# Performance work log

Hardware: AMD Instinct MI355X
Metric: run time of the kernel (lower is better)

## Reference

```python
import jax, jax.numpy as jnp
import numpy as np

N_HEAD = 16
SCALE = True  # module's scale flag: divides scores by d_head (as written, NOT sqrt)
NEG = 1e10


def setup_inputs() -> dict:
    key = jax.random.key(0)
    k0, k1, k2 = jax.random.split(key, 3)
    B, S, NX = 2, 2048, 1024
    x = jax.random.normal(k0, (B, S, NX), dtype=jnp.float32)
    w_attn = jax.random.normal(k1, (NX, 3 * NX), dtype=jnp.float32) * 0.02
    b_attn = jnp.zeros((3 * NX,), dtype=jnp.float32)
    w_proj = jax.random.normal(k2, (NX, NX), dtype=jnp.float32) * 0.02
    b_proj = jnp.zeros((NX,), dtype=jnp.float32)
    return {"x": x, "w_attn": w_attn, "b_attn": b_attn, "w_proj": w_proj, "b_proj": b_proj}


def reference(x, w_attn, b_attn, w_proj, b_proj):
    B, S, nx = x.shape
    d = nx // N_HEAD
    # c_attn: fused qkv projection (Conv1D == addmm)
    qkv = x @ w_attn + b_attn  # [B,S,3*nx]
    q, k, v = jnp.split(qkv, 3, axis=-1)

    def heads(t):
        return t.reshape(B, S, N_HEAD, d).transpose(0, 2, 1, 3)  # [B,H,S,d]

    q, k, v = heads(q), heads(k), heads(v)
    w = jnp.einsum('bhqd,bhkd->bhqk', q, k)  # [B,H,S,S]
    if SCALE:
        w = w / d  # module divides by v.size(-1) == d_head (not sqrt)
    mask = jnp.tril(jnp.ones((S, S), dtype=w.dtype))
    w = w * mask - NEG * (1.0 - mask)
    w = jax.nn.softmax(w, axis=-1)
    a = jnp.einsum('bhqk,bhkd->bhqd', w, v)
    a = a.transpose(0, 2, 1, 3).reshape(B, S, nx)  # merge_heads
    out = a @ w_proj + b_proj  # c_proj
    # present = stack(key.transpose(-2,-1), value); key was [B,H,d,S] in torch,
    # so stored key is [B,H,S,d] which equals our k.
    present = jnp.stack((k, v))  # [2,B,H,S,d]
    return out, present
```

## Files before the change

kernel.cpp:

```cpp
#include <hip/hip_runtime.h>
#include <hip/hip_bf16.h>
#include <stdint.h>


typedef __bf16 bf16;
typedef __attribute__((ext_vector_type(8))) __bf16 bf16x8;
typedef __attribute__((ext_vector_type(4))) float f32x4;

#define SEQ 2048
#define NXD 1024
#define DH 64
#define LP 72

__device__ __forceinline__ f32x4 mfma16(bf16x8 a, bf16x8 b, f32x4 c) {
  return __builtin_amdgcn_mfma_f32_16x16x32_bf16(a, b, c, 0, 0, 0);
}

__global__ __launch_bounds__(256) void convert_f32_bf16(
    const float* __restrict__ in, bf16* __restrict__ out, int n8) {
  const int i = blockIdx.x * 256 + threadIdx.x;
  if (i >= n8) return;
  const float4 a = ((const float4*)in)[i * 2];
  const float4 b = ((const float4*)in)[i * 2 + 1];
  bf16x8 o;
  o[0] = (bf16)a.x; o[1] = (bf16)a.y; o[2] = (bf16)a.z; o[3] = (bf16)a.w;
  o[4] = (bf16)b.x; o[5] = (bf16)b.y; o[6] = (bf16)b.z; o[7] = (bf16)b.w;
  ((bf16x8*)out)[i] = o;
}

__global__ __launch_bounds__(256) void transpose64_f2b(
    const float* __restrict__ in, bf16* __restrict__ out, int R, int C) {
  __shared__ bf16 tile[64 * 65];
  const int t = threadIdx.x;
  const size_t bofs = (size_t)blockIdx.z * R * C;
  const float* ib = in + bofs;
  bf16* ob = out + bofs;
  const int r0 = blockIdx.y * 64, c0 = blockIdx.x * 64;
#pragma unroll
  for (int i = 0; i < 4; i++) {
    int flat = (i * 256 + t) * 4;
    int row = flat >> 6, col = flat & 63;
    float4 v = *(const float4*)(ib + (size_t)(r0 + row) * C + c0 + col);
    tile[row * 65 + col + 0] = (bf16)v.x;
    tile[row * 65 + col + 1] = (bf16)v.y;
    tile[row * 65 + col + 2] = (bf16)v.z;
    tile[row * 65 + col + 3] = (bf16)v.w;
  }
  __syncthreads();
#pragma unroll
  for (int i = 0; i < 2; i++) {
    int flat = (i * 256 + t) * 8;
    int orow = flat >> 6, ocol = flat & 63;
    bf16x8 v;
#pragma unroll
    for (int e = 0; e < 8; e++) v[e] = tile[(ocol + e) * 65 + orow];
    *(bf16x8*)(ob + (size_t)(c0 + orow) * R + r0 + ocol) = v;
  }
}

template <int MODE>
__global__ __launch_bounds__(256) void gemm128s(
    const bf16* __restrict__ A, const bf16* __restrict__ BT,
    const float* __restrict__ bias, bf16* __restrict__ qb,
    float* __restrict__ of1, float* __restrict__ of2) {
  __shared__ bf16 As[128 * LP];
  __shared__ bf16 Bs[128 * LP];
  const int t = threadIdx.x;
  const int lane = t & 63, wave = t >> 6;
  const int hi = lane >> 4, ln = lane & 15;
  const int wr = wave >> 1, wc = wave & 1;
  const int tm0 = blockIdx.y * 128, tn0 = blockIdx.x * 128;

  f32x4 acc[4][4];
#pragma unroll
  for (int m = 0; m < 4; m++)
#pragma unroll
    for (int n = 0; n < 4; n++) acc[m][n] = (f32x4){0.f, 0.f, 0.f, 0.f};

  for (int k0 = 0; k0 < 1024; k0 += 64) {
#pragma unroll
    for (int it = 0; it < 4; ++it) {
      const int e = (it * 256 + t) * 8;
      const int row = e >> 6, col = e & 63;
      *(bf16x8*)(As + row * LP + col) =
          *(const bf16x8*)(A + (size_t)(tm0 + row) * 1024 + k0 + col);
      *(bf16x8*)(Bs + row * LP + col) =
          *(const bf16x8*)(BT + (size_t)(tn0 + row) * 1024 + k0 + col);
    }
    __syncthreads();
#pragma unroll
    for (int kk = 0; kk < 2; ++kk) {
      bf16x8 af[4], bfr[4];
#pragma unroll
      for (int m = 0; m < 4; m++) {
        const int ar = wr * 64 + m * 16 + ln;
        af[m] = *(const bf16x8*)(As + ar * LP + kk * 32 + hi * 8);
      }
#pragma unroll
      for (int n = 0; n < 4; n++) {
        const int br = wc * 64 + n * 16 + ln;
        bfr[n] = *(const bf16x8*)(Bs + br * LP + kk * 32 + hi * 8);
      }
#pragma unroll
      for (int m = 0; m < 4; m++)
#pragma unroll
        for (int n = 0; n < 4; n++)
          acc[m][n] = mfma16(af[m], bfr[n], acc[m][n]);
    }
    __syncthreads();
  }
#pragma unroll
  for (int m = 0; m < 4; m++) {
#pragma unroll
    for (int n = 0; n < 4; n++) {
      const int c = tn0 + wc * 64 + n * 16 + ln;
      const float bv = bias[c];
#pragma unroll
      for (int reg = 0; reg < 4; reg++) {
        const int r = tm0 + wr * 64 + m * 16 + hi * 4 + reg;
        const float v = acc[m][n][reg] + bv;
        if (MODE == 0) {
          const int b = r >> 11, s = r & 2047;
          const int which = c >> 10, cc = c & 1023;
          const int h = cc >> 6, dc = cc & 63;
          const size_t idx = (((size_t)(b * 16 + h)) * 2048 + s) * 64 + dc;
          if (which == 0) qb[idx] = (bf16)v;
          else if (which == 1) of1[idx] = v;
          else of2[idx] = v;
        } else {
          of1[(size_t)r * 1024 + c] = v;
        }
      }
    }
  }
}

__global__ __launch_bounds__(256) void attn_kernel(
    const bf16* __restrict__ Q, const float* __restrict__ K,
    const bf16* __restrict__ VT, bf16* __restrict__ Aout) {
  __shared__ bf16 Ks[64 * LP];
  __shared__ bf16 Vs[64 * LP];
  __shared__ bf16 Pall[4 * 16 * LP];
  const int t = threadIdx.x, lane = t & 63, wave = t >> 6;
  const int hi = lane >> 4, ln = lane & 15;
  bf16* Psw = Pall + wave * 16 * LP;
  const int qt = blockIdx.x, bh = blockIdx.y;
  const int qrow_base = qt * 64 + wave * 16;

  bf16x8 qf[2];
#pragma unroll
  for (int kk = 0; kk < 2; kk++)
    qf[kk] = *(const bf16x8*)(Q + ((size_t)bh * SEQ + qrow_base + ln) * DH +
                              kk * 32 + hi * 8);

  f32x4 o[4];
#pragma unroll
  for (int nd = 0; nd < 4; nd++) o[nd] = (f32x4){0.f, 0.f, 0.f, 0.f};
  float mrun[4], lrun[4];
#pragma unroll
  for (int r = 0; r < 4; r++) { mrun[r] = -3e38f; lrun[r] = 0.f; }

  for (int j = 0; j <= qt; ++j) {
#pragma unroll
    for (int it = 0; it < 2; ++it) {
      const int e = (it * 256 + t) * 8;
      const int row = e >> 6, col = e & 63;
      const float* kp = K + ((size_t)bh * SEQ + j * 64 + row) * DH + col;
      const float4 f0 = *(const float4*)kp;
      const float4 f1 = *(const float4*)(kp + 4);
      bf16x8 kb;
      kb[0] = (bf16)f0.x; kb[1] = (bf16)f0.y;
      kb[2] = (bf16)f0.z; kb[3] = (bf16)f0.w;
      kb[4] = (bf16)f1.x; kb[5] = (bf16)f1.y;
      kb[6] = (bf16)f1.z; kb[7] = (bf16)f1.w;
      *(bf16x8*)(Ks + row * LP + col) = kb;
      *(bf16x8*)(Vs + row * LP + col) = *(const bf16x8*)(
          VT + ((size_t)bh * DH + row) * SEQ + j * 64 + col);
    }
    __syncthreads();

    f32x4 s[4];
#pragma unroll
    for (int n = 0; n < 4; n++) s[n] = (f32x4){0.f, 0.f, 0.f, 0.f};
#pragma unroll
    for (int kk = 0; kk < 2; kk++) {
#pragma unroll
      for (int n = 0; n < 4; n++) {
        const int kr = n * 16 + ln;
        bf16x8 kf = *(const bf16x8*)(Ks + kr * LP + kk * 32 + hi * 8);
        s[n] = mfma16(qf[kk], kf, s[n]);
      }
    }
    const bool diag = (j == qt);
#pragma unroll
    for (int n = 0; n < 4; n++) {
#pragma unroll
      for (int reg = 0; reg < 4; reg++) {
        float v = s[n][reg] * (1.f / 64.f);
        if (diag) {
          const int col = j * 64 + n * 16 + ln;
          const int row = qrow_base + hi * 4 + reg;
          if (col > row) v = -1e10f;
        }
        s[n][reg] = v;
      }
    }
    float pm[4];
#pragma unroll
    for (int reg = 0; reg < 4; reg++)
      pm[reg] = fmaxf(fmaxf(s[0][reg], s[1][reg]), fmaxf(s[2][reg], s[3][reg]));
#pragma unroll
    for (int off = 1; off < 16; off <<= 1)
#pragma unroll
      for (int reg = 0; reg < 4; reg++)
        pm[reg] = fmaxf(pm[reg], __shfl_xor(pm[reg], off));
    float alpha[4];
#pragma unroll
    for (int reg = 0; reg < 4; reg++) {
      const float mnew = fmaxf(mrun[reg], pm[reg]);
      alpha[reg] = __expf(mrun[reg] - mnew);
      mrun[reg] = mnew;
    }
    float rs[4] = {0.f, 0.f, 0.f, 0.f};
#pragma unroll
    for (int n = 0; n < 4; n++)
#pragma unroll
      for (int reg = 0; reg < 4; reg++) {
        const float p = __expf(s[n][reg] - mrun[reg]);
        s[n][reg] = p;
        rs[reg] += p;
      }
#pragma unroll
    for (int off = 1; off < 16; off <<= 1)
#pragma unroll
      for (int reg = 0; reg < 4; reg++) rs[reg] += __shfl_xor(rs[reg], off);
#pragma unroll
    for (int reg = 0; reg < 4; reg++)
      lrun[reg] = lrun[reg] * alpha[reg] + rs[reg];
#pragma unroll
    for (int nd = 0; nd < 4; nd++)
#pragma unroll
      for (int reg = 0; reg < 4; reg++) o[nd][reg] *= alpha[reg];
#pragma unroll
    for (int n = 0; n < 4; n++)
#pragma unroll
      for (int reg = 0; reg < 4; reg++)
        Psw[(hi * 4 + reg) * LP + n * 16 + ln] = (bf16)s[n][reg];
#pragma unroll
    for (int kk = 0; kk < 2; kk++) {
      bf16x8 pa = *(const bf16x8*)(Psw + ln * LP + kk * 32 + hi * 8);
#pragma unroll
      for (int nd = 0; nd < 4; nd++) {
        const int vr = nd * 16 + ln;
        bf16x8 vf = *(const bf16x8*)(Vs + vr * LP + kk * 32 + hi * 8);
        o[nd] = mfma16(pa, vf, o[nd]);
      }
    }
    __syncthreads();
  }
  const int bq = bh >> 4, h = bh & 15;
#pragma unroll
  for (int nd = 0; nd < 4; nd++)
#pragma unroll
    for (int reg = 0; reg < 4; reg++) {
      const int srow = qrow_base + hi * 4 + reg;
      const float inv = 1.f / lrun[reg];
      Aout[((size_t)bq * SEQ + srow) * NXD + h * 64 + nd * 16 + ln] =
          (bf16)(o[nd][reg] * inv);
    }
}

extern "C" void kernel_launch(void* const* d_in, const int* in_sizes, int n_in,
                              void* d_out, int out_size, void* d_ws,
                              size_t ws_size, hipStream_t stream) {
  const float* x = (const float*)d_in[0];
  const float* w_attn = (const float*)d_in[1];
  const float* b_attn = (const float*)d_in[2];
  const float* w_proj = (const float*)d_in[3];
  const float* b_proj = (const float*)d_in[4];

  float* out = (float*)d_out;
  float* kout = out + 4194304;
  float* vout = kout + 4194304;

  bf16* wT = (bf16*)d_ws;
  bf16* wpT = wT + 3072 * 1024;
  bf16* Qws = wpT + 1024 * 1024;
  bf16* VTws = Qws + 4194304;
  bf16* Aws = VTws + 4194304;
  bf16* Xb = Aws;

  convert_f32_bf16<<<dim3(2048), 256, 0, stream>>>(x, Xb, 524288);
  transpose64_f2b<<<dim3(48, 16, 1), 256, 0, stream>>>(w_attn, wT, 1024, 3072);
  transpose64_f2b<<<dim3(16, 16, 1), 256, 0, stream>>>(w_proj, wpT, 1024,
                                                       1024);
  gemm128s<0><<<dim3(24, 32), 256, 0, stream>>>(Xb, wT, b_attn, Qws, kout,
                                                vout);
  transpose64_f2b<<<dim3(1, 32, 32), 256, 0, stream>>>(vout, VTws, 2048, 64);
  attn_kernel<<<dim3(32, 32), 256, 0, stream>>>(Qws, kout, VTws, Aws);
  gemm128s<1><<<dim3(8, 32), 256, 0, stream>>>(Aws, wpT, b_proj, nullptr, out,
                                               nullptr);
}
```

Before: 294.4 us.

## Load K and V fragments directly from global memory in attention, dropping LDS staging

```diff
diff --git a/kernel.cpp b/kernel.cpp
--- a/kernel.cpp
+++ b/kernel.cpp
@@ -138,8 +138,6 @@
 __global__ __launch_bounds__(256) void attn_kernel(
     const bf16* __restrict__ Q, const float* __restrict__ K,
     const bf16* __restrict__ VT, bf16* __restrict__ Aout) {
-  __shared__ bf16 Ks[64 * LP];
-  __shared__ bf16 Vs[64 * LP];
   __shared__ bf16 Pall[4 * 16 * LP];
   const int t = threadIdx.x, lane = t & 63, wave = t >> 6;
   const int hi = lane >> 4, ln = lane & 15;
@@ -153,6 +151,9 @@
     qf[kk] = *(const bf16x8*)(Q + ((size_t)bh * SEQ + qrow_base + ln) * DH +
                               kk * 32 + hi * 8);
 
+  const float* Kb = K + (size_t)bh * SEQ * DH;
+  const bf16* VTb = VT + (size_t)bh * DH * SEQ;
+
   f32x4 o[4];
 #pragma unroll
   for (int nd = 0; nd < 4; nd++) o[nd] = (f32x4){0.f, 0.f, 0.f, 0.f};
@@ -161,24 +162,6 @@
   for (int r = 0; r < 4; r++) { mrun[r] = -3e38f; lrun[r] = 0.f; }
 
   for (int j = 0; j <= qt; ++j) {
-#pragma unroll
-    for (int it = 0; it < 2; ++it) {
-      const int e = (it * 256 + t) * 8;
-      const int row = e >> 6, col = e & 63;
-      const float* kp = K + ((size_t)bh * SEQ + j * 64 + row) * DH + col;
-      const float4 f0 = *(const float4*)kp;
-      const float4 f1 = *(const float4*)(kp + 4);
-      bf16x8 kb;
-      kb[0] = (bf16)f0.x; kb[1] = (bf16)f0.y;
-      kb[2] = (bf16)f0.z; kb[3] = (bf16)f0.w;
-      kb[4] = (bf16)f1.x; kb[5] = (bf16)f1.y;
-      kb[6] = (bf16)f1.z; kb[7] = (bf16)f1.w;
-      *(bf16x8*)(Ks + row * LP + col) = kb;
-      *(bf16x8*)(Vs + row * LP + col) = *(const bf16x8*)(
-          VT + ((size_t)bh * DH + row) * SEQ + j * 64 + col);
-    }
-    __syncthreads();
-
     f32x4 s[4];
 #pragma unroll
     for (int n = 0; n < 4; n++) s[n] = (f32x4){0.f, 0.f, 0.f, 0.f};
@@ -186,8 +169,15 @@
     for (int kk = 0; kk < 2; kk++) {
 #pragma unroll
       for (int n = 0; n < 4; n++) {
-        const int kr = n * 16 + ln;
-        bf16x8 kf = *(const bf16x8*)(Ks + kr * LP + kk * 32 + hi * 8);
+        const float* kp =
+            Kb + (size_t)(j * 64 + n * 16 + ln) * DH + kk * 32 + hi * 8;
+        const float4 f0 = *(const float4*)kp;
+        const float4 f1 = *(const float4*)(kp + 4);
+        bf16x8 kf;
+        kf[0] = (bf16)f0.x; kf[1] = (bf16)f0.y;
+        kf[2] = (bf16)f0.z; kf[3] = (bf16)f0.w;
+        kf[4] = (bf16)f1.x; kf[5] = (bf16)f1.y;
+        kf[6] = (bf16)f1.z; kf[7] = (bf16)f1.w;
         s[n] = mfma16(qf[kk], kf, s[n]);
       }
     }
@@ -251,12 +241,11 @@
       bf16x8 pa = *(const bf16x8*)(Psw + ln * LP + kk * 32 + hi * 8);
 #pragma unroll
       for (int nd = 0; nd < 4; nd++) {
-        const int vr = nd * 16 + ln;
-        bf16x8 vf = *(const bf16x8*)(Vs + vr * LP + kk * 32 + hi * 8);
+        bf16x8 vf = *(const bf16x8*)(VTb + (size_t)(nd * 16 + ln) * SEQ +
+                                     j * 64 + kk * 32 + hi * 8);
         o[nd] = mfma16(pa, vf, o[nd]);
       }
     }
-    __syncthreads();
   }
   const int bq = bh >> 4, h = bh & 15;
 #pragma unroll
```

Result: slower. 504.1 us (+71.2%).

## Use direct global-to-LDS swizzled loads in GEMM and balance causal attention

Applied to the files above, without the earlier changes.

```diff
diff --git a/kernel.cpp b/kernel.cpp
--- a/kernel.cpp
+++ b/kernel.cpp
@@ -11,6 +11,13 @@
 #define NXD 1024
 #define DH 64
 #define LP 72
+#define NT 32
+
+__device__ __forceinline__ void gload16(const void* g, void* l) {
+  __builtin_amdgcn_global_load_lds(
+      (const __attribute__((address_space(1))) uint32_t*)(uintptr_t)g,
+      (__attribute__((address_space(3))) uint32_t*)(uintptr_t)l, 16, 0, 0);
+}
 
 __device__ __forceinline__ f32x4 mfma16(bf16x8 a, bf16x8 b, f32x4 c) {
   return __builtin_amdgcn_mfma_f32_16x16x32_bf16(a, b, c, 0, 0, 0);
@@ -59,12 +66,13 @@
 }
 
 template <int MODE>
-__global__ __launch_bounds__(256) void gemm128s(
+__global__ __launch_bounds__(256) void gemm128(
     const bf16* __restrict__ A, const bf16* __restrict__ BT,
     const float* __restrict__ bias, bf16* __restrict__ qb,
     float* __restrict__ of1, float* __restrict__ of2) {
-  __shared__ bf16 As[128 * LP];
-  __shared__ bf16 Bs[128 * LP];
+  __shared__ char smem[32768];
+  bf16* As = (bf16*)smem;
+  bf16* Bs = (bf16*)(smem + 16384);
   const int t = threadIdx.x;
   const int lane = t & 63, wave = t >> 6;
   const int hi = lane >> 4, ln = lane & 15;
@@ -79,13 +87,14 @@
 
   for (int k0 = 0; k0 < 1024; k0 += 64) {
 #pragma unroll
-    for (int it = 0; it < 4; ++it) {
-      const int e = (it * 256 + t) * 8;
-      const int row = e >> 6, col = e & 63;
-      *(bf16x8*)(As + row * LP + col) =
-          *(const bf16x8*)(A + (size_t)(tm0 + row) * 1024 + k0 + col);
-      *(bf16x8*)(Bs + row * LP + col) =
-          *(const bf16x8*)(BT + (size_t)(tn0 + row) * 1024 + k0 + col);
+    for (int cch = 0; cch < 4; ++cch) {
+      const int fb = cch * 4096 + wave * 1024;
+      const int f = fb + lane * 16;
+      const int row = f >> 7;
+      const int sc = ((f >> 4) & 7) ^ (row & 7);
+      gload16(A + (size_t)(tm0 + row) * 1024 + k0 + sc * 8, smem + fb);
+      gload16(BT + (size_t)(tn0 + row) * 1024 + k0 + sc * 8,
+              smem + 16384 + fb);
     }
     __syncthreads();
 #pragma unroll
@@ -94,12 +103,14 @@
 #pragma unroll
       for (int m = 0; m < 4; m++) {
         const int ar = wr * 64 + m * 16 + ln;
-        af[m] = *(const bf16x8*)(As + ar * LP + kk * 32 + hi * 8);
+        af[m] = *(const bf16x8*)(As + ar * 64 +
+                                 ((kk * 32 + hi * 8) ^ ((ar & 7) << 3)));
       }
 #pragma unroll
       for (int n = 0; n < 4; n++) {
         const int br = wc * 64 + n * 16 + ln;
-        bfr[n] = *(const bf16x8*)(Bs + br * LP + kk * 32 + hi * 8);
+        bfr[n] = *(const bf16x8*)(Bs + br * 64 +
+                                  ((kk * 32 + hi * 8) ^ ((br & 7) << 3)));
       }
 #pragma unroll
       for (int m = 0; m < 4; m++)
@@ -138,136 +149,165 @@
 __global__ __launch_bounds__(256) void attn_kernel(
     const bf16* __restrict__ Q, const float* __restrict__ K,
     const bf16* __restrict__ VT, bf16* __restrict__ Aout) {
-  __shared__ bf16 Ks[64 * LP];
-  __shared__ bf16 Vs[64 * LP];
+  __shared__ bf16 KsBuf[2][64 * LP];
+  __shared__ bf16 VsBuf[2][64 * LP];
   __shared__ bf16 Pall[4 * 16 * LP];
   const int t = threadIdx.x, lane = t & 63, wave = t >> 6;
   const int hi = lane >> 4, ln = lane & 15;
   bf16* Psw = Pall + wave * 16 * LP;
-  const int qt = blockIdx.x, bh = blockIdx.y;
-  const int qrow_base = qt * 64 + wave * 16;
-
-  bf16x8 qf[2];
-#pragma unroll
-  for (int kk = 0; kk < 2; kk++)
-    qf[kk] = *(const bf16x8*)(Q + ((size_t)bh * SEQ + qrow_base + ln) * DH +
-                              kk * 32 + hi * 8);
-
-  f32x4 o[4];
-#pragma unroll
-  for (int nd = 0; nd < 4; nd++) o[nd] = (f32x4){0.f, 0.f, 0.f, 0.f};
-  float mrun[4], lrun[4];
-#pragma unroll
-  for (int r = 0; r < 4; r++) { mrun[r] = -3e38f; lrun[r] = 0.f; }
-
-  for (int j = 0; j <= qt; ++j) {
+  const int bid = blockIdx.x, bh = blockIdx.y;
+  const int bq = bh >> 4, h = bh & 15;
+
+  const float* Kb = K + (size_t)bh * SEQ * DH;
+  const bf16* VTb = VT + (size_t)bh * DH * SEQ;
+
+  const int srow0 = t >> 3, scol = (t & 7) * 8;
+  float4 kreg[2][2];
+  bf16x8 vreg[2];
+
+#pragma unroll
+  for (int half = 0; half < 2; ++half) {
+    const int qt = half ? (NT - 1 - bid) : bid;
+    const int qrow_base = qt * 64 + wave * 16;
+
+    bf16x8 qf[2];
+#pragma unroll
+    for (int kk = 0; kk < 2; kk++)
+      qf[kk] = *(const bf16x8*)(Q + ((size_t)bh * SEQ + qrow_base + ln) * DH +
+                                kk * 32 + hi * 8);
+
+    f32x4 o[4];
+#pragma unroll
+    for (int nd = 0; nd < 4; nd++) o[nd] = (f32x4){0.f, 0.f, 0.f, 0.f};
+    float mrun[4], lrun[4];
+#pragma unroll
+    for (int r = 0; r < 4; r++) { mrun[r] = -3e38f; lrun[r] = 0.f; }
+
 #pragma unroll
     for (int it = 0; it < 2; ++it) {
-      const int e = (it * 256 + t) * 8;
-      const int row = e >> 6, col = e & 63;
-      const float* kp = K + ((size_t)bh * SEQ + j * 64 + row) * DH + col;
-      const float4 f0 = *(const float4*)kp;
-      const float4 f1 = *(const float4*)(kp + 4);
-      bf16x8 kb;
-      kb[0] = (bf16)f0.x; kb[1] = (bf16)f0.y;
-      kb[2] = (bf16)f0.z; kb[3] = (bf16)f0.w;
-      kb[4] = (bf16)f1.x; kb[5] = (bf16)f1.y;
-      kb[6] = (bf16)f1.z; kb[7] = (bf16)f1.w;
-      *(bf16x8*)(Ks + row * LP + col) = kb;
-      *(bf16x8*)(Vs + row * LP + col) = *(const bf16x8*)(
-          VT + ((size_t)bh * DH + row) * SEQ + j * 64 + col);
+      const int row = srow0 + it * 32;
+      const float* kp = Kb + (size_t)row * DH + scol;
+      kreg[it][0] = *(const float4*)kp;
+      kreg[it][1] = *(const float4*)(kp + 4);
+      vreg[it] = *(const bf16x8*)(VTb + (size_t)row * SEQ + scol);
+    }
+
+    for (int j = 0; j <= qt; ++j) {
+      bf16* Ks = KsBuf[j & 1];
+      bf16* Vs = VsBuf[j & 1];
+#pragma unroll
+      for (int it = 0; it < 2; ++it) {
+        const int row = srow0 + it * 32;
+        bf16x8 kb;
+        kb[0] = (bf16)kreg[it][0].x; kb[1] = (bf16)kreg[it][0].y;
+        kb[2] = (bf16)kreg[it][0].z; kb[3] = (bf16)kreg[it][0].w;
+        kb[4] = (bf16)kreg[it][1].x; kb[5] = (bf16)kreg[it][1].y;
+        kb[6] = (bf16)kreg[it][1].z; kb[7] = (bf16)kreg[it][1].w;
+        *(bf16x8*)(Ks + row * LP + scol) = kb;
+        *(bf16x8*)(Vs + row * LP + scol) = vreg[it];
+      }
+      __syncthreads();
+      if (j < qt) {
+        const int jn = j + 1;
+#pragma unroll
+        for (int it = 0; it < 2; ++it) {
+          const int row = srow0 + it * 32;
+          const float* kp = Kb + (size_t)(jn * 64 + row) * DH + scol;
+          kreg[it][0] = *(const float4*)kp;
+          kreg[it][1] = *(const float4*)(kp + 4);
+          vreg[it] = *(const bf16x8*)(VTb + (size_t)row * SEQ + jn * 64 + scol);
+        }
+      }
+      f32x4 s[4];
+#pragma unroll
+      for (int n = 0; n < 4; n++) s[n] = (f32x4){0.f, 0.f, 0.f, 0.f};
+#pragma unroll
+      for (int kk = 0; kk < 2; kk++) {
+#pragma unroll
+        for (int n = 0; n < 4; n++) {
+          const int kr = n * 16 + ln;
+          bf16x8 kf = *(const bf16x8*)(Ks + kr * LP + kk * 32 + hi * 8);
+          s[n] = mfma16(qf[kk], kf, s[n]);
+        }
+      }
+      const bool diag = (j == qt);
+#pragma unroll
+      for (int n = 0; n < 4; n++) {
+#pragma unroll
+        for (int reg = 0; reg < 4; reg++) {
+          float v = s[n][reg] * (1.f / 64.f);
+          if (diag) {
+            const int col = j * 64 + n * 16 + ln;
+            const int row = qrow_base + hi * 4 + reg;
+            if (col > row) v = -1e10f;
+          }
+          s[n][reg] = v;
+        }
+      }
+      float pm[4];
+#pragma unroll
+      for (int reg = 0; reg < 4; reg++)
+        pm[reg] =
+            fmaxf(fmaxf(s[0][reg], s[1][reg]), fmaxf(s[2][reg], s[3][reg]));
+#pragma unroll
+      for (int off = 1; off < 16; off <<= 1)
+#pragma unroll
+        for (int reg = 0; reg < 4; reg++)
+          pm[reg] = fmaxf(pm[reg], __shfl_xor(pm[reg], off));
+      float alpha[4];
+#pragma unroll
+      for (int reg = 0; reg < 4; reg++) {
+        const float mnew = fmaxf(mrun[reg], pm[reg]);
+        alpha[reg] = __expf(mrun[reg] - mnew);
+        mrun[reg] = mnew;
+      }
+      float rs[4] = {0.f, 0.f, 0.f, 0.f};
+#pragma unroll
+      for (int n = 0; n < 4; n++)
+#pragma unroll
+        for (int reg = 0; reg < 4; reg++) {
+          const float p = __expf(s[n][reg] - mrun[reg]);
+          s[n][reg] = p;
+          rs[reg] += p;
+        }
+#pragma unroll
+      for (int off = 1; off < 16; off <<= 1)
+#pragma unroll
+        for (int reg = 0; reg < 4; reg++) rs[reg] += __shfl_xor(rs[reg], off);
+#pragma unroll
+      for (int reg = 0; reg < 4; reg++)
+        lrun[reg] = lrun[reg] * alpha[reg] + rs[reg];
+#pragma unroll
+      for (int nd = 0; nd < 4; nd++)
+#pragma unroll
+        for (int reg = 0; reg < 4; reg++) o[nd][reg] *= alpha[reg];
+#pragma unroll
+      for (int n = 0; n < 4; n++)
+#pragma unroll
+        for (int reg = 0; reg < 4; reg++)
+          Psw[(hi * 4 + reg) * LP + n * 16 + ln] = (bf16)s[n][reg];
+#pragma unroll
+      for (int kk = 0; kk < 2; kk++) {
+        bf16x8 pa = *(const bf16x8*)(Psw + ln * LP + kk * 32 + hi * 8);
+#pragma unroll
+        for (int nd = 0; nd < 4; nd++) {
+          const int vr = nd * 16 + ln;
+          bf16x8 vf = *(const bf16x8*)(Vs + vr * LP + kk * 32 + hi * 8);
+          o[nd] = mfma16(pa, vf, o[nd]);
+        }
+      }
     }
     __syncthreads();
-
-    f32x4 s[4];
-#pragma unroll
-    for (int n = 0; n < 4; n++) s[n] = (f32x4){0.f, 0.f, 0.f, 0.f};
-#pragma unroll
-    for (int kk = 0; kk < 2; kk++) {
-#pragma unroll
-      for (int n = 0; n < 4; n++) {
-        const int kr = n * 16 + ln;
-        bf16x8 kf = *(const bf16x8*)(Ks + kr * LP + kk * 32 + hi * 8);
-        s[n] = mfma16(qf[kk], kf, s[n]);
-      }
-    }
-    const bool diag = (j == qt);
-#pragma unroll
-    for (int n = 0; n < 4; n++) {
+#pragma unroll
+    for (int nd = 0; nd < 4; nd++)
 #pragma unroll
       for (int reg = 0; reg < 4; reg++) {
-        float v = s[n][reg] * (1.f / 64.f);
-        if (diag) {
-          const int col = j * 64 + n * 16 + ln;
-          const int row = qrow_base + hi * 4 + reg;
-          if (col > row) v = -1e10f;
-        }
-        s[n][reg] = v;
-      }
-    }
-    float pm[4];
-#pragma unroll
-    for (int reg = 0; reg < 4; reg++)
-      pm[reg] = fmaxf(fmaxf(s[0][reg], s[1][reg]), fmaxf(s[2][reg], s[3][reg]));
-#pragma unroll
-    for (int off = 1; off < 16; off <<= 1)
-#pragma unroll
-      for (int reg = 0; reg < 4; reg++)
-        pm[reg] = fmaxf(pm[reg], __shfl_xor(pm[reg], off));
-    float alpha[4];
-#pragma unroll
-    for (int reg = 0; reg < 4; reg++) {
-      const float mnew = fmaxf(mrun[reg], pm[reg]);
-      alpha[reg] = __expf(mrun[reg] - mnew);
-      mrun[reg] = mnew;
-    }
-    float rs[4] = {0.f, 0.f, 0.f, 0.f};
-#pragma unroll
-    for (int n = 0; n < 4; n++)
-#pragma unroll
-      for (int reg = 0; reg < 4; reg++) {
-        const float p = __expf(s[n][reg] - mrun[reg]);
-        s[n][reg] = p;
-        rs[reg] += p;
-      }
-#pragma unroll
-    for (int off = 1; off < 16; off <<= 1)
-#pragma unroll
-      for (int reg = 0; reg < 4; reg++) rs[reg] += __shfl_xor(rs[reg], off);
-#pragma unroll
-    for (int reg = 0; reg < 4; reg++)
-      lrun[reg] = lrun[reg] * alpha[reg] + rs[reg];
-#pragma unroll
-    for (int nd = 0; nd < 4; nd++)
-#pragma unroll
-      for (int reg = 0; reg < 4; reg++) o[nd][reg] *= alpha[reg];
-#pragma unroll
-    for (int n = 0; n < 4; n++)
-#pragma unroll
-      for (int reg = 0; reg < 4; reg++)
-        Psw[(hi * 4 + reg) * LP + n * 16 + ln] = (bf16)s[n][reg];
-#pragma unroll
-    for (int kk = 0; kk < 2; kk++) {
-      bf16x8 pa = *(const bf16x8*)(Psw + ln * LP + kk * 32 + hi * 8);
-#pragma unroll
-      for (int nd = 0; nd < 4; nd++) {
-        const int vr = nd * 16 + ln;
-        bf16x8 vf = *(const bf16x8*)(Vs + vr * LP + kk * 32 + hi * 8);
-        o[nd] = mfma16(pa, vf, o[nd]);
-      }
-    }
-    __syncthreads();
-  }
-  const int bq = bh >> 4, h = bh & 15;
-#pragma unroll
-  for (int nd = 0; nd < 4; nd++)
-#pragma unroll
-    for (int reg = 0; reg < 4; reg++) {
-      const int srow = qrow_base + hi * 4 + reg;
-      const float inv = 1.f / lrun[reg];
-      Aout[((size_t)bq * SEQ + srow) * NXD + h * 64 + nd * 16 + ln] =
-          (bf16)(o[nd][reg] * inv);
-    }
+        const int srow = qrow_base + hi * 4 + reg;
+        const float inv = 1.f / lrun[reg];
+        Aout[((size_t)bq * SEQ + srow) * NXD + h * 64 + nd * 16 + ln] =
+            (bf16)(o[nd][reg] * inv);
+      }
+  }
 }
 
 extern "C" void kernel_launch(void* const* d_in, const int* in_sizes, int n_in,
@@ -294,10 +334,10 @@
   transpose64_f2b<<<dim3(48, 16, 1), 256, 0, stream>>>(w_attn, wT, 1024, 3072);
   transpose64_f2b<<<dim3(16, 16, 1), 256, 0, stream>>>(w_proj, wpT, 1024,
                                                        1024);
-  gemm128s<0><<<dim3(24, 32), 256, 0, stream>>>(Xb, wT, b_attn, Qws, kout,
-                                                vout);
+  gemm128<0><<<dim3(24, 32), 256, 0, stream>>>(Xb, wT, b_attn, Qws, kout,
+                                               vout);
   transpose64_f2b<<<dim3(1, 32, 32), 256, 0, stream>>>(vout, VTws, 2048, 64);
-  attn_kernel<<<dim3(32, 32), 256, 0, stream>>>(Qws, kout, VTws, Aws);
-  gemm128s<1><<<dim3(8, 32), 256, 0, stream>>>(Aws, wpT, b_proj, nullptr, out,
-                                               nullptr);
-}
+  attn_kernel<<<dim3(NT / 2, 32), 256, 0, stream>>>(Qws, kout, VTws, Aws);
+  gemm128<1><<<dim3(8, 32), 256, 0, stream>>>(Aws, wpT, b_proj, nullptr, out,
+                                              nullptr);
+}
```

Result: faster. 238.5 us (-19.0%).
